# Kernel optimization log

Measured on AMD Instinct MI355X. Metric: run time of the kernel, lower is better.

## Reference

```python
import jax, jax.numpy as jnp
import numpy as np

OUT_F, IN_F = 4096, 11008
NUMEL = OUT_F * IN_F            # divisible by 256
NUM_SUPER = NUMEL // 256        # super-blocks of 8 sub-blocks x 32 values


def setup_inputs() -> dict:
    key = jax.random.key(0)
    k = jax.random.split(key, 7)
    x = jax.random.normal(k[0], (64, IN_F), dtype=jnp.float32)
    packed = jax.random.randint(k[1], (NUMEL // 2,), 0, 256, dtype=jnp.int32)
    d = jax.random.uniform(k[2], (NUM_SUPER,), dtype=jnp.float32) * 0.02
    dmin = jax.random.uniform(k[3], (NUM_SUPER,), dtype=jnp.float32) * 0.02
    scales = jax.random.randint(k[4], (NUM_SUPER * 8,), 0, 64, dtype=jnp.int32)
    mins = jax.random.randint(k[5], (NUM_SUPER * 8,), 0, 64, dtype=jnp.int32)
    bias = jax.random.normal(k[6], (OUT_F,), dtype=jnp.float32) * 0.02
    return {"x": x, "packed": packed, "d": d, "dmin": dmin,
            "scales": scales, "mins": mins, "bias": bias}


def _dequant_q4k(packed, d, dmin, scales, mins):
    # unpack two 4-bit quants per byte, interleaved low/high (stack dim=1 + flatten)
    low = packed & 15
    high = (packed >> 4) & 15
    q = jnp.stack([low, high], axis=1).reshape(NUM_SUPER, 8, 32).astype(jnp.float32)
    sc = (scales.astype(jnp.float32) / 63.0).reshape(NUM_SUPER, 8, 1)
    mn = (mins.astype(jnp.float32) / 63.0).reshape(NUM_SUPER, 8, 1)
    normalized = q / 15.0 * sc + mn
    w = normalized * d.reshape(NUM_SUPER, 1, 1) + dmin.reshape(NUM_SUPER, 1, 1)
    return w.reshape(OUT_F, IN_F)


def reference(x, packed, d, dmin, scales, mins, bias):
    w = _dequant_q4k(packed, d, dmin, scales, mins)   # [OUT_F, IN_F] fp32
    return x @ w.T + bias                              # F.linear
```

## Files before the change

kernel.cpp:

```cpp
#include <hip/hip_runtime.h>
#include <stdint.h>

#define OUT_F   4096
#define IN_F    11008
#define BATCH   64
#define NSUP    43
#define SB_ROW  344
#define IPR     5504
#define NKS     12
#define XP_BYTES   (4 * 344 * 64 * 16)
#define PART_ELEMS ((size_t)NKS * BATCH * OUT_F)
#define WS_FULL    (XP_BYTES + PART_ELEMS * 4)

typedef __attribute__((ext_vector_type(8))) short  short8;
typedef __attribute__((ext_vector_type(4))) float  floatx4;
typedef __attribute__((ext_vector_type(4))) int    intx4;

template<int N> struct IC { static constexpr int value = N; };

__device__ __forceinline__ unsigned pack_bf16(float f0, float f1) {
    return __builtin_amdgcn_perm(__float_as_uint(f1), __float_as_uint(f0), 0x07060302u);
}

__device__ __forceinline__ void glds16(const void* g, void* s) {
    __builtin_amdgcn_global_load_lds(
        (const __attribute__((address_space(1))) uint32_t*)g,
        (__attribute__((address_space(3))) uint32_t*)s,
        16, 0, 0);
}

__device__ __forceinline__ void wait_vm0(void) {
    asm volatile("s_waitcnt vmcnt(0)" ::: "memory");
    __builtin_amdgcn_sched_barrier(0);
}

__global__ __launch_bounds__(256) void xprep_kernel(const float* __restrict__ x,
                                                    intx4* __restrict__ xp) {
    const int ksb = blockIdx.x;
    const int mt  = threadIdx.x >> 6;
    const int l   = threadIdx.x & 63;
    const int lo  = l & 15, hi = l >> 4;
    const float* src = x + (mt * 16 + lo) * IN_F + ksb * 32 + hi * 8;
    floatx4 a0 = *(const floatx4*)src;
    floatx4 a1 = *(const floatx4*)(src + 4);
    intx4 r;
    r.x = pack_bf16(a0.x, a0.y);
    r.y = pack_bf16(a0.z, a0.w);
    r.z = pack_bf16(a1.x, a1.y);
    r.w = pack_bf16(a1.z, a1.w);
    xp[(mt * 344 + ksb) * 64 + l] = r;
}

__global__ __launch_bounds__(256) void init_out_kernel(const float* __restrict__ bias,
                                                       float* __restrict__ out) {
    int i = blockIdx.x * 256 + threadIdx.x;
    out[i] = bias[i & (OUT_F - 1)];
}

__global__ __launch_bounds__(256) void reduce_kernel(const float* __restrict__ part,
                                                     const float* __restrict__ bias,
                                                     float* __restrict__ out) {
    const int i = blockIdx.x * 256 + threadIdx.x;
    float s = bias[i & (OUT_F - 1)];
    #pragma unroll
    for (int k = 0; k < NKS; ++k) s += part[(size_t)k * (BATCH * OUT_F) + i];
    out[i] = s;
}

template<bool USE_PART>
__global__ __launch_bounds__(256, 3) void qlin_main(
    const intx4* __restrict__ xp,
    const int*   __restrict__ packed,
    const float* __restrict__ dd,
    const float* __restrict__ dmn_g,
    const int*   __restrict__ scales,
    const int*   __restrict__ mins,
    float*       __restrict__ part,
    float*       __restrict__ out)
{
    __shared__ intx4 xfs[2048];

    const int nb  = blockIdx.x & 63;
    const int ks  = blockIdx.x >> 6;
    const int tid = threadIdx.x;
    const int w   = tid >> 6;
    const int l   = tid & 63;
    const int lo  = l & 15, hi = l >> 4;
    const int wq  = tid & 192;

    const int o    = nb * 64 + w * 16 + lo;
    const int sup0 = ks < 7 ? 4 * ks : 28 + 3 * (ks - 7);
    const int nsup = ks < 7 ? 4 : 3;

    floatx4 acc[4];
    #pragma unroll
    for (int mt = 0; mt < 4; ++mt) acc[mt] = (floatx4)0.0f;

    const int*   bp0 = packed + o * IPR + sup0 * 128 + hi * 4;
    const int*   scp = scales + o * SB_ROW + sup0 * 8;
    const int*   mnp = mins   + o * SB_ROW + sup0 * 8;
    const float* dp  = dd     + o * NSUP + sup0;
    const float* dmp = dmn_g  + o * NSUP + sup0;

    auto stage_x = [&](int sup_abs) {
        #pragma unroll
        for (int i = 0; i < 8; ++i) {
            const int mt = i >> 1;
            const intx4* src = xp + sup_abs * 512 + mt * 22016 + (i & 1) * 256 + tid;
            glds16((const void*)src, (void*)&xfs[i * 256 + wq]);
        }
    };

    auto load_wblk = [&](int s, intx4 br[8], intx4& s0v, intx4& s1v,
                         intx4& m0v, intx4& m1v, float& dv, float& dmv) {
        #pragma unroll
        for (int st = 0; st < 8; ++st)
            br[st] = __builtin_nontemporal_load((const intx4*)(bp0 + s * 128 + st * 16));
        s0v = *(const intx4*)(scp + s * 8);
        s1v = *(const intx4*)(scp + s * 8 + 4);
        m0v = *(const intx4*)(mnp + s * 8);
        m1v = *(const intx4*)(mnp + s * 8 + 4);
        dv  = dp[s];
        dmv = dmp[s];
    };

    auto compute_sup = [&](const intx4 br[8], intx4 s0v, intx4 s1v,
                           intx4 m0v, intx4 m1v, float dv, float dmv) {
        const float A945 = dv * (1.0f / 945.0f);
        const float A63  = dv * (1.0f / 63.0f);
        #pragma unroll
        for (int st = 0; st < 8; ++st) {
            const int scv = (st < 4) ? s0v[st & 3] : s1v[st & 3];
            const int mnv = (st < 4) ? m0v[st & 3] : m1v[st & 3];
            const float A = A945 * (float)scv;
            const float B = fmaf(A63, (float)mnv, dmv);
            const int v0 = br[st].x, v1 = br[st].y, v2 = br[st].z, v3 = br[st].w;
            union { intx4 i; short8 s8; } uw;
            uw.i.x = pack_bf16(fmaf((float)(v0 & 15), A, B), fmaf((float)(v0 >> 4), A, B));
            uw.i.y = pack_bf16(fmaf((float)(v1 & 15), A, B), fmaf((float)(v1 >> 4), A, B));
            uw.i.z = pack_bf16(fmaf((float)(v2 & 15), A, B), fmaf((float)(v2 >> 4), A, B));
            uw.i.w = pack_bf16(fmaf((float)(v3 & 15), A, B), fmaf((float)(v3 >> 4), A, B));

            union { intx4 i; short8 s8; } u0, u1, u2, u3;
            u0.i = xfs[0 * 512 + st * 64 + l];
            u1.i = xfs[1 * 512 + st * 64 + l];
            u2.i = xfs[2 * 512 + st * 64 + l];
            u3.i = xfs[3 * 512 + st * 64 + l];
            acc[0] = __builtin_amdgcn_mfma_f32_16x16x32_bf16(u0.s8, uw.s8, acc[0], 0, 0, 0);
            acc[1] = __builtin_amdgcn_mfma_f32_16x16x32_bf16(u1.s8, uw.s8, acc[1], 0, 0, 0);
            acc[2] = __builtin_amdgcn_mfma_f32_16x16x32_bf16(u2.s8, uw.s8, acc[2], 0, 0, 0);
            acc[3] = __builtin_amdgcn_mfma_f32_16x16x32_bf16(u3.s8, uw.s8, acc[3], 0, 0, 0);
        }
    };

    auto run = [&](auto nsc) {
        constexpr int NS = decltype(nsc)::value;
        intx4 br[8]; intx4 s0v, s1v, m0v, m1v; float dv, dmv;

        load_wblk(0, br, s0v, s1v, m0v, m1v, dv, dmv);
        stage_x(sup0);
        wait_vm0();
        __builtin_amdgcn_s_barrier();

        #pragma unroll
        for (int s = 0; s < NS; ++s) {
            intx4 brN[8]; intx4 s0N, s1N, m0N, m1N; float dvN, dmvN;
            if (s + 1 < NS)
                load_wblk(s + 1, brN, s0N, s1N, m0N, m1N, dvN, dmvN);

            compute_sup(br, s0v, s1v, m0v, m1v, dv, dmv);

            if (s + 1 < NS) {
                __builtin_amdgcn_s_barrier();
                stage_x(sup0 + s + 1);
                wait_vm0();
                __builtin_amdgcn_s_barrier();
                #pragma unroll
                for (int i2 = 0; i2 < 8; ++i2) br[i2] = brN[i2];
                s0v = s0N; s1v = s1N; m0v = m0N; m1v = m1N; dv = dvN; dmv = dmvN;
            }
        }
    };
    if (nsup == 4) run(IC<4>{});
    else           run(IC<3>{});

    if (USE_PART) {
        float* pbase = part + (size_t)ks * (BATCH * OUT_F) + o;
        #pragma unroll
        for (int mt = 0; mt < 4; ++mt) {
            #pragma unroll
            for (int rr = 0; rr < 4; ++rr)
                pbase[(mt * 16 + hi * 4 + rr) * OUT_F] = acc[mt][rr];
        }
    } else {
        #pragma unroll
        for (int mt = 0; mt < 4; ++mt) {
            #pragma unroll
            for (int rr = 0; rr < 4; ++rr)
                atomicAdd(out + (mt * 16 + hi * 4 + rr) * OUT_F + o, acc[mt][rr]);
        }
    }
}

extern "C" void kernel_launch(void* const* d_in, const int* in_sizes, int n_in,
                              void* d_out, int out_size, void* d_ws, size_t ws_size,
                              hipStream_t stream) {
    (void)in_sizes; (void)n_in; (void)out_size;
    const float* x      = (const float*)d_in[0];
    const int*   packed = (const int*)d_in[1];
    const float* d      = (const float*)d_in[2];
    const float* dmin   = (const float*)d_in[3];
    const int*   scales = (const int*)d_in[4];
    const int*   mins   = (const int*)d_in[5];
    const float* bias   = (const float*)d_in[6];
    float* out = (float*)d_out;

    const bool has_part = ws_size >= (size_t)WS_FULL;
    intx4* xp   = (intx4*)d_ws;
    float* part = (float*)((char*)d_ws + XP_BYTES);

    xprep_kernel<<<344, 256, 0, stream>>>(x, xp);

    if (has_part) {
        qlin_main<true><<<64 * NKS, 256, 0, stream>>>(
            xp, packed, d, dmin, scales, mins, part, out);
        reduce_kernel<<<(BATCH * OUT_F) / 256, 256, 0, stream>>>(part, bias, out);
    } else {
        init_out_kernel<<<(BATCH * OUT_F) / 256, 256, 0, stream>>>(bias, out);
        qlin_main<false><<<64 * NKS, 256, 0, stream>>>(
            xp, packed, d, dmin, scales, mins, part, out);
    }
}
```

Baseline: 168.5 us.

## Fuse x bf16 conversion into main kernel and drop software pipelining

Removes the separate xprep kernel. Each block now loads fp32 x directly, converts it to bf16 in registers and writes it to LDS, instead of async-copying a pre-packed bf16 buffer. The prefetch of the next super-block's weights is also dropped, so loads and compute run sequentially within each iteration. This saves one kernel launch and the workspace round trip, but every one of the 64 column blocks now reads twice the x bytes (fp32), and the weight-load latency is no longer overlapped with compute.

New measurement: 183.0 us. +8.6%, slower.

```diff
diff --git a/kernel.cpp b/kernel.cpp
--- a/kernel.cpp
+++ b/kernel.cpp
@@ -8,9 +8,8 @@
 #define SB_ROW  344
 #define IPR     5504
 #define NKS     12
-#define XP_BYTES   (4 * 344 * 64 * 16)
 #define PART_ELEMS ((size_t)NKS * BATCH * OUT_F)
-#define WS_FULL    (XP_BYTES + PART_ELEMS * 4)
+#define WS_FULL    (PART_ELEMS * 4)
 
 typedef __attribute__((ext_vector_type(8))) short  short8;
 typedef __attribute__((ext_vector_type(4))) float  floatx4;
@@ -20,35 +19,6 @@
 
 __device__ __forceinline__ unsigned pack_bf16(float f0, float f1) {
     return __builtin_amdgcn_perm(__float_as_uint(f1), __float_as_uint(f0), 0x07060302u);
-}
-
-__device__ __forceinline__ void glds16(const void* g, void* s) {
-    __builtin_amdgcn_global_load_lds(
-        (const __attribute__((address_space(1))) uint32_t*)g,
-        (__attribute__((address_space(3))) uint32_t*)s,
-        16, 0, 0);
-}
-
-__device__ __forceinline__ void wait_vm0(void) {
-    asm volatile("s_waitcnt vmcnt(0)" ::: "memory");
-    __builtin_amdgcn_sched_barrier(0);
-}
-
-__global__ __launch_bounds__(256) void xprep_kernel(const float* __restrict__ x,
-                                                    intx4* __restrict__ xp) {
-    const int ksb = blockIdx.x;
-    const int mt  = threadIdx.x >> 6;
-    const int l   = threadIdx.x & 63;
-    const int lo  = l & 15, hi = l >> 4;
-    const float* src = x + (mt * 16 + lo) * IN_F + ksb * 32 + hi * 8;
-    floatx4 a0 = *(const floatx4*)src;
-    floatx4 a1 = *(const floatx4*)(src + 4);
-    intx4 r;
-    r.x = pack_bf16(a0.x, a0.y);
-    r.y = pack_bf16(a0.z, a0.w);
-    r.z = pack_bf16(a1.x, a1.y);
-    r.w = pack_bf16(a1.z, a1.w);
-    xp[(mt * 344 + ksb) * 64 + l] = r;
 }
 
 __global__ __launch_bounds__(256) void init_out_kernel(const float* __restrict__ bias,
@@ -69,7 +39,7 @@
 
 template<bool USE_PART>
 __global__ __launch_bounds__(256, 3) void qlin_main(
-    const intx4* __restrict__ xp,
+    const float* __restrict__ x,
     const int*   __restrict__ packed,
     const float* __restrict__ dd,
     const float* __restrict__ dmn_g,
@@ -86,7 +56,6 @@
     const int w   = tid >> 6;
     const int l   = tid & 63;
     const int lo  = l & 15, hi = l >> 4;
-    const int wq  = tid & 192;
 
     const int o    = nb * 64 + w * 16 + lo;
     const int sup0 = ks < 7 ? 4 * ks : 28 + 3 * (ks - 7);
@@ -102,82 +71,77 @@
     const float* dp  = dd     + o * NSUP + sup0;
     const float* dmp = dmn_g  + o * NSUP + sup0;
 
-    auto stage_x = [&](int sup_abs) {
-        #pragma unroll
-        for (int i = 0; i < 8; ++i) {
-            const int mt = i >> 1;
-            const intx4* src = xp + sup_abs * 512 + mt * 22016 + (i & 1) * 256 + tid;
-            glds16((const void*)src, (void*)&xfs[i * 256 + wq]);
-        }
-    };
-
-    auto load_wblk = [&](int s, intx4 br[8], intx4& s0v, intx4& s1v,
-                         intx4& m0v, intx4& m1v, float& dv, float& dmv) {
-        #pragma unroll
-        for (int st = 0; st < 8; ++st)
-            br[st] = __builtin_nontemporal_load((const intx4*)(bp0 + s * 128 + st * 16));
-        s0v = *(const intx4*)(scp + s * 8);
-        s1v = *(const intx4*)(scp + s * 8 + 4);
-        m0v = *(const intx4*)(mnp + s * 8);
-        m1v = *(const intx4*)(mnp + s * 8 + 4);
-        dv  = dp[s];
-        dmv = dmp[s];
-    };
-
-    auto compute_sup = [&](const intx4 br[8], intx4 s0v, intx4 s1v,
-                           intx4 m0v, intx4 m1v, float dv, float dmv) {
-        const float A945 = dv * (1.0f / 945.0f);
-        const float A63  = dv * (1.0f / 63.0f);
-        #pragma unroll
-        for (int st = 0; st < 8; ++st) {
-            const int scv = (st < 4) ? s0v[st & 3] : s1v[st & 3];
-            const int mnv = (st < 4) ? m0v[st & 3] : m1v[st & 3];
-            const float A = A945 * (float)scv;
-            const float B = fmaf(A63, (float)mnv, dmv);
-            const int v0 = br[st].x, v1 = br[st].y, v2 = br[st].z, v3 = br[st].w;
-            union { intx4 i; short8 s8; } uw;
-            uw.i.x = pack_bf16(fmaf((float)(v0 & 15), A, B), fmaf((float)(v0 >> 4), A, B));
-            uw.i.y = pack_bf16(fmaf((float)(v1 & 15), A, B), fmaf((float)(v1 >> 4), A, B));
-            uw.i.z = pack_bf16(fmaf((float)(v2 & 15), A, B), fmaf((float)(v2 >> 4), A, B));
-            uw.i.w = pack_bf16(fmaf((float)(v3 & 15), A, B), fmaf((float)(v3 >> 4), A, B));
-
-            union { intx4 i; short8 s8; } u0, u1, u2, u3;
-            u0.i = xfs[0 * 512 + st * 64 + l];
-            u1.i = xfs[1 * 512 + st * 64 + l];
-            u2.i = xfs[2 * 512 + st * 64 + l];
-            u3.i = xfs[3 * 512 + st * 64 + l];
-            acc[0] = __builtin_amdgcn_mfma_f32_16x16x32_bf16(u0.s8, uw.s8, acc[0], 0, 0, 0);
-            acc[1] = __builtin_amdgcn_mfma_f32_16x16x32_bf16(u1.s8, uw.s8, acc[1], 0, 0, 0);
-            acc[2] = __builtin_amdgcn_mfma_f32_16x16x32_bf16(u2.s8, uw.s8, acc[2], 0, 0, 0);
-            acc[3] = __builtin_amdgcn_mfma_f32_16x16x32_bf16(u3.s8, uw.s8, acc[3], 0, 0, 0);
-        }
-    };
+    int xoff[8];
+    #pragma unroll
+    for (int i = 0; i < 8; ++i) {
+        const int n  = i * 256 + tid;
+        const int mt = n >> 9;
+        const int st2 = (n >> 6) & 7;
+        const int l2 = n & 63;
+        xoff[i] = (mt * 16 + (l2 & 15)) * IN_F + st2 * 32 + (l2 >> 4) * 8;
+    }
 
     auto run = [&](auto nsc) {
         constexpr int NS = decltype(nsc)::value;
-        intx4 br[8]; intx4 s0v, s1v, m0v, m1v; float dv, dmv;
-
-        load_wblk(0, br, s0v, s1v, m0v, m1v, dv, dmv);
-        stage_x(sup0);
-        wait_vm0();
-        __builtin_amdgcn_s_barrier();
-
         #pragma unroll
         for (int s = 0; s < NS; ++s) {
-            intx4 brN[8]; intx4 s0N, s1N, m0N, m1N; float dvN, dmvN;
-            if (s + 1 < NS)
-                load_wblk(s + 1, brN, s0N, s1N, m0N, m1N, dvN, dmvN);
+            const int sup = sup0 + s;
 
-            compute_sup(br, s0v, s1v, m0v, m1v, dv, dmv);
+            intx4 br[8];
+            #pragma unroll
+            for (int st = 0; st < 8; ++st)
+                br[st] = __builtin_nontemporal_load((const intx4*)(bp0 + s * 128 + st * 16));
+            const intx4 s0v = *(const intx4*)(scp + s * 8);
+            const intx4 s1v = *(const intx4*)(scp + s * 8 + 4);
+            const intx4 m0v = *(const intx4*)(mnp + s * 8);
+            const intx4 m1v = *(const intx4*)(mnp + s * 8 + 4);
+            const float dv  = dp[s];
+            const float dmv = dmp[s];
 
-            if (s + 1 < NS) {
-                __builtin_amdgcn_s_barrier();
-                stage_x(sup0 + s + 1);
-                wait_vm0();
-                __builtin_amdgcn_s_barrier();
-                #pragma unroll
-                for (int i2 = 0; i2 < 8; ++i2) br[i2] = brN[i2];
-                s0v = s0N; s1v = s1N; m0v = m0N; m1v = m1N; dv = dvN; dmv = dmvN;
+            intx4 xt[8];
+            #pragma unroll
+            for (int i = 0; i < 8; ++i) {
+                const float* src = x + xoff[i] + sup * 256;
+                floatx4 a0 = *(const floatx4*)src;
+                floatx4 a1 = *(const floatx4*)(src + 4);
+                xt[i].x = pack_bf16(a0.x, a0.y);
+                xt[i].y = pack_bf16(a0.z, a0.w);
+                xt[i].z = pack_bf16(a1.x, a1.y);
+                xt[i].w = pack_bf16(a1.z, a1.w);
+            }
+
+            if (s > 0) __builtin_amdgcn_s_barrier();
+            #pragma unroll
+            for (int i = 0; i < 8; ++i)
+                xfs[i * 256 + tid] = xt[i];
+            asm volatile("s_waitcnt lgkmcnt(0)" ::: "memory");
+            __builtin_amdgcn_sched_barrier(0);
+            __builtin_amdgcn_s_barrier();
+
+            const float A945 = dv * (1.0f / 945.0f);
+            const float A63  = dv * (1.0f / 63.0f);
+            #pragma unroll
+            for (int st = 0; st < 8; ++st) {
+                const int scv = (st < 4) ? s0v[st & 3] : s1v[st & 3];
+                const int mnv = (st < 4) ? m0v[st & 3] : m1v[st & 3];
+                const float A = A945 * (float)scv;
+                const float B = fmaf(A63, (float)mnv, dmv);
+                const int v0 = br[st].x, v1 = br[st].y, v2 = br[st].z, v3 = br[st].w;
+                union { intx4 i; short8 s8; } uw;
+                uw.i.x = pack_bf16(fmaf((float)(v0 & 15), A, B), fmaf((float)(v0 >> 4), A, B));
+                uw.i.y = pack_bf16(fmaf((float)(v1 & 15), A, B), fmaf((float)(v1 >> 4), A, B));
+                uw.i.z = pack_bf16(fmaf((float)(v2 & 15), A, B), fmaf((float)(v2 >> 4), A, B));
+                uw.i.w = pack_bf16(fmaf((float)(v3 & 15), A, B), fmaf((float)(v3 >> 4), A, B));
+
+                union { intx4 i; short8 s8; } u0, u1, u2, u3;
+                u0.i = xfs[0 * 512 + st * 64 + l];
+                u1.i = xfs[1 * 512 + st * 64 + l];
+                u2.i = xfs[2 * 512 + st * 64 + l];
+                u3.i = xfs[3 * 512 + st * 64 + l];
+                acc[0] = __builtin_amdgcn_mfma_f32_16x16x32_bf16(u0.s8, uw.s8, acc[0], 0, 0, 0);
+                acc[1] = __builtin_amdgcn_mfma_f32_16x16x32_bf16(u1.s8, uw.s8, acc[1], 0, 0, 0);
+                acc[2] = __builtin_amdgcn_mfma_f32_16x16x32_bf16(u2.s8, uw.s8, acc[2], 0, 0, 0);
+                acc[3] = __builtin_amdgcn_mfma_f32_16x16x32_bf16(u3.s8, uw.s8, acc[3], 0, 0, 0);
             }
         }
     };
@@ -216,18 +180,15 @@
     float* out = (float*)d_out;
 
     const bool has_part = ws_size >= (size_t)WS_FULL;
-    intx4* xp   = (intx4*)d_ws;
-    float* part = (float*)((char*)d_ws + XP_BYTES);
-
-    xprep_kernel<<<344, 256, 0, stream>>>(x, xp);
+    float* part = (float*)d_ws;
 
     if (has_part) {
         qlin_main<true><<<64 * NKS, 256, 0, stream>>>(
-            xp, packed, d, dmin, scales, mins, part, out);
+            x, packed, d, dmin, scales, mins, part, out);
         reduce_kernel<<<(BATCH * OUT_F) / 256, 256, 0, stream>>>(part, bias, out);
     } else {
         init_out_kernel<<<(BATCH * OUT_F) / 256, 256, 0, stream>>>(bias, out);
         qlin_main<false><<<64 * NKS, 256, 0, stream>>>(
-            xp, packed, d, dmin, scales, mins, part, out);
+            x, packed, d, dmin, scales, mins, part, out);
     }
 }
```

## Double-buffer x tiles and prefetch weights two super-blocks ahead with fewer K splits

Applied to the files above, without the earlier changes.

The LDS x tile becomes double-buffered, and weight blocks are prefetched two super-blocks ahead into register arrays. The full vmcnt(0) drain per step is replaced by a partial s_waitcnt vmcnt(22), so the next group's loads stay in flight during compute. The K split drops from 12 to 8, giving each block 5–6 super-blocks and shrinking the partial-sum buffer and the reduction, and occupancy is lowered to 2 blocks per CU. The hardcoded vmcnt count assumes exactly 22 memory ops per group, which breaks if the compiler merges or splits loads, and the extra register and LDS use may limit latency hiding.

Measured after the change: 166.1 us. Within noise of the previous version (-1.4%).

```diff
diff --git a/kernel.cpp b/kernel.cpp
--- a/kernel.cpp
+++ b/kernel.cpp
@@ -7,7 +7,7 @@
 #define NSUP    43
 #define SB_ROW  344
 #define IPR     5504
-#define NKS     12
+#define NKS     8
 #define XP_BYTES   (4 * 344 * 64 * 16)
 #define PART_ELEMS ((size_t)NKS * BATCH * OUT_F)
 #define WS_FULL    (XP_BYTES + PART_ELEMS * 4)
@@ -29,8 +29,8 @@
         16, 0, 0);
 }
 
-__device__ __forceinline__ void wait_vm0(void) {
-    asm volatile("s_waitcnt vmcnt(0)" ::: "memory");
+__device__ __forceinline__ void group_fence(void) {
+    asm volatile("" ::: "memory");
     __builtin_amdgcn_sched_barrier(0);
 }
 
@@ -68,7 +68,7 @@
 }
 
 template<bool USE_PART>
-__global__ __launch_bounds__(256, 3) void qlin_main(
+__global__ __launch_bounds__(256, 2) void qlin_main(
     const intx4* __restrict__ xp,
     const int*   __restrict__ packed,
     const float* __restrict__ dd,
@@ -78,7 +78,7 @@
     float*       __restrict__ part,
     float*       __restrict__ out)
 {
-    __shared__ intx4 xfs[2048];
+    __shared__ intx4 xfs[2][2048];
 
     const int nb  = blockIdx.x & 63;
     const int ks  = blockIdx.x >> 6;
@@ -89,8 +89,8 @@
     const int wq  = tid & 192;
 
     const int o    = nb * 64 + w * 16 + lo;
-    const int sup0 = ks < 7 ? 4 * ks : 28 + 3 * (ks - 7);
-    const int nsup = ks < 7 ? 4 : 3;
+    const int sup0 = ks < 3 ? 6 * ks : 18 + 5 * (ks - 3);
+    const int nsup = ks < 3 ? 6 : 5;
 
     floatx4 acc[4];
     #pragma unroll
@@ -102,87 +102,86 @@
     const float* dp  = dd     + o * NSUP + sup0;
     const float* dmp = dmn_g  + o * NSUP + sup0;
 
-    auto stage_x = [&](int sup_abs) {
+    auto stage_x = [&](int sup_abs, int buf) {
         #pragma unroll
         for (int i = 0; i < 8; ++i) {
-            const int mt = i >> 1;
-            const intx4* src = xp + sup_abs * 512 + mt * 22016 + (i & 1) * 256 + tid;
-            glds16((const void*)src, (void*)&xfs[i * 256 + wq]);
-        }
-    };
-
-    auto load_wblk = [&](int s, intx4 br[8], intx4& s0v, intx4& s1v,
-                         intx4& m0v, intx4& m1v, float& dv, float& dmv) {
-        #pragma unroll
-        for (int st = 0; st < 8; ++st)
-            br[st] = __builtin_nontemporal_load((const intx4*)(bp0 + s * 128 + st * 16));
-        s0v = *(const intx4*)(scp + s * 8);
-        s1v = *(const intx4*)(scp + s * 8 + 4);
-        m0v = *(const intx4*)(mnp + s * 8);
-        m1v = *(const intx4*)(mnp + s * 8 + 4);
-        dv  = dp[s];
-        dmv = dmp[s];
-    };
-
-    auto compute_sup = [&](const intx4 br[8], intx4 s0v, intx4 s1v,
-                           intx4 m0v, intx4 m1v, float dv, float dmv) {
-        const float A945 = dv * (1.0f / 945.0f);
-        const float A63  = dv * (1.0f / 63.0f);
-        #pragma unroll
-        for (int st = 0; st < 8; ++st) {
-            const int scv = (st < 4) ? s0v[st & 3] : s1v[st & 3];
-            const int mnv = (st < 4) ? m0v[st & 3] : m1v[st & 3];
-            const float A = A945 * (float)scv;
-            const float B = fmaf(A63, (float)mnv, dmv);
-            const int v0 = br[st].x, v1 = br[st].y, v2 = br[st].z, v3 = br[st].w;
-            union { intx4 i; short8 s8; } uw;
-            uw.i.x = pack_bf16(fmaf((float)(v0 & 15), A, B), fmaf((float)(v0 >> 4), A, B));
-            uw.i.y = pack_bf16(fmaf((float)(v1 & 15), A, B), fmaf((float)(v1 >> 4), A, B));
-            uw.i.z = pack_bf16(fmaf((float)(v2 & 15), A, B), fmaf((float)(v2 >> 4), A, B));
-            uw.i.w = pack_bf16(fmaf((float)(v3 & 15), A, B), fmaf((float)(v3 >> 4), A, B));
-
-            union { intx4 i; short8 s8; } u0, u1, u2, u3;
-            u0.i = xfs[0 * 512 + st * 64 + l];
-            u1.i = xfs[1 * 512 + st * 64 + l];
-            u2.i = xfs[2 * 512 + st * 64 + l];
-            u3.i = xfs[3 * 512 + st * 64 + l];
-            acc[0] = __builtin_amdgcn_mfma_f32_16x16x32_bf16(u0.s8, uw.s8, acc[0], 0, 0, 0);
-            acc[1] = __builtin_amdgcn_mfma_f32_16x16x32_bf16(u1.s8, uw.s8, acc[1], 0, 0, 0);
-            acc[2] = __builtin_amdgcn_mfma_f32_16x16x32_bf16(u2.s8, uw.s8, acc[2], 0, 0, 0);
-            acc[3] = __builtin_amdgcn_mfma_f32_16x16x32_bf16(u3.s8, uw.s8, acc[3], 0, 0, 0);
+            const intx4* src = xp + (i >> 1) * 22016 + sup_abs * 512 + (i & 1) * 256 + tid;
+            glds16((const void*)src, (void*)&xfs[buf][i * 256 + wq]);
         }
     };
 
     auto run = [&](auto nsc) {
         constexpr int NS = decltype(nsc)::value;
-        intx4 br[8]; intx4 s0v, s1v, m0v, m1v; float dv, dmv;
-
-        load_wblk(0, br, s0v, s1v, m0v, m1v, dv, dmv);
-        stage_x(sup0);
-        wait_vm0();
-        __builtin_amdgcn_s_barrier();
+        intx4 br[NS][8];
+        intx4 s0[NS], s1[NS], m0[NS], m1[NS];
+        float dv[NS], dmv[NS];
+
+        auto issue_w = [&](int s) {
+            #pragma unroll
+            for (int st = 0; st < 8; ++st)
+                br[s][st] = __builtin_nontemporal_load((const intx4*)(bp0 + s * 128 + st * 16));
+            s0[s]  = *(const intx4*)(scp + s * 8);
+            s1[s]  = *(const intx4*)(scp + s * 8 + 4);
+            m0[s]  = *(const intx4*)(mnp + s * 8);
+            m1[s]  = *(const intx4*)(mnp + s * 8 + 4);
+            dv[s]  = dp[s];
+            dmv[s] = dmp[s];
+        };
+
+        auto compute_sup = [&](int s, int buf) {
+            const float A945 = dv[s] * (1.0f / 945.0f);
+            const float A63  = dv[s] * (1.0f / 63.0f);
+            #pragma unroll
+            for (int st = 0; st < 8; ++st) {
+                const int scv = (st < 4) ? s0[s][st & 3] : s1[s][st & 3];
+                const int mnv = (st < 4) ? m0[s][st & 3] : m1[s][st & 3];
+                const float A = A945 * (float)scv;
+                const float B = fmaf(A63, (float)mnv, dmv[s]);
+                const int v0 = br[s][st].x, v1 = br[s][st].y;
+                const int v2 = br[s][st].z, v3 = br[s][st].w;
+                union { intx4 i; short8 s8; } uw;
+                uw.i.x = pack_bf16(fmaf((float)(v0 & 15), A, B), fmaf((float)(v0 >> 4), A, B));
+                uw.i.y = pack_bf16(fmaf((float)(v1 & 15), A, B), fmaf((float)(v1 >> 4), A, B));
+                uw.i.z = pack_bf16(fmaf((float)(v2 & 15), A, B), fmaf((float)(v2 >> 4), A, B));
+                uw.i.w = pack_bf16(fmaf((float)(v3 & 15), A, B), fmaf((float)(v3 >> 4), A, B));
+
+                union { intx4 i; short8 s8; } u0, u1, u2, u3;
+                u0.i = xfs[buf][0 * 512 + st * 64 + l];
+                u1.i = xfs[buf][1 * 512 + st * 64 + l];
+                u2.i = xfs[buf][2 * 512 + st * 64 + l];
+                u3.i = xfs[buf][3 * 512 + st * 64 + l];
+                acc[0] = __builtin_amdgcn_mfma_f32_16x16x32_bf16(u0.s8, uw.s8, acc[0], 0, 0, 0);
+                acc[1] = __builtin_amdgcn_mfma_f32_16x16x32_bf16(u1.s8, uw.s8, acc[1], 0, 0, 0);
+                acc[2] = __builtin_amdgcn_mfma_f32_16x16x32_bf16(u2.s8, uw.s8, acc[2], 0, 0, 0);
+                acc[3] = __builtin_amdgcn_mfma_f32_16x16x32_bf16(u3.s8, uw.s8, acc[3], 0, 0, 0);
+            }
+        };
+
+        issue_w(0); stage_x(sup0 + 0, 0);
+        group_fence();
+        issue_w(1); stage_x(sup0 + 1, 1);
+        group_fence();
 
         #pragma unroll
         for (int s = 0; s < NS; ++s) {
-            intx4 brN[8]; intx4 s0N, s1N, m0N, m1N; float dvN, dmvN;
-            if (s + 1 < NS)
-                load_wblk(s + 1, brN, s0N, s1N, m0N, m1N, dvN, dmvN);
-
-            compute_sup(br, s0v, s1v, m0v, m1v, dv, dmv);
-
-            if (s + 1 < NS) {
+            if (s + 1 < NS) asm volatile("s_waitcnt vmcnt(22)" ::: "memory");
+            else            asm volatile("s_waitcnt vmcnt(0)"  ::: "memory");
+            __builtin_amdgcn_sched_barrier(0);
+            __builtin_amdgcn_s_barrier();
+
+            if (s + 2 < NS) issue_w(s + 2);
+
+            compute_sup(s, s & 1);
+
+            if (s + 2 < NS) {
                 __builtin_amdgcn_s_barrier();
-                stage_x(sup0 + s + 1);
-                wait_vm0();
-                __builtin_amdgcn_s_barrier();
-                #pragma unroll
-                for (int i2 = 0; i2 < 8; ++i2) br[i2] = brN[i2];
-                s0v = s0N; s1v = s1N; m0v = m0N; m1v = m1N; dv = dvN; dmv = dmvN;
+                stage_x(sup0 + s + 2, s & 1);
+                group_fence();
             }
         }
     };
-    if (nsup == 4) run(IC<4>{});
-    else           run(IC<3>{});
+    if (nsup == 6) run(IC<6>{});
+    else           run(IC<5>{});
 
     if (USE_PART) {
         float* pbase = part + (size_t)ks * (BATCH * OUT_F) + o;
```
